# Performance work log

Hardware: AMD Instinct MI355X
Metric: run time of the kernel (lower is better)

## Reference

```python
import jax, jax.numpy as jnp
import numpy as np
from jax import lax

FEAT = 384        # features
FFN = 768         # ffn_features (chunk=True -> halves of 384)
ZDIM = FFN // 2   # 384
HID = 192         # AE hidden
B, N = 4, 128
LN_EPS = 1e-5


def gelu(x):
    return jax.nn.gelu(x, approximate=False)  # torch nn.GELU default = exact erf


def setup_inputs() -> dict:
    key = jax.random.key(0)
    ks = jax.random.split(key, 12)

    def lin(k, fan_in, shape):
        bound = 1.0 / np.sqrt(fan_in)
        return jax.random.uniform(k, shape, jnp.float32, -bound, bound)

    return {
        "x": jax.random.normal(ks[0], (B, N, FEAT), jnp.float32),
        "U_w": lin(ks[1], FEAT, (FEAT, FFN)),
        "U_b": lin(ks[2], FEAT, (FFN,)),
        "ln_w": jnp.ones((ZDIM,), jnp.float32),
        "ln_b": jnp.zeros((ZDIM,), jnp.float32),
        "enc_w": lin(ks[3], ZDIM, (ZDIM, HID)),
        "enc_b": lin(ks[4], ZDIM, (HID,)),
        "dec_w": lin(ks[5], HID, (HID, ZDIM)),
        "dec_b": lin(ks[6], HID, (ZDIM,)),
        "V_w": lin(ks[7], ZDIM, (ZDIM, FEAT)),
        "V_b": lin(ks[8], ZDIM, (FEAT,)),
    }


def _ae(z, enc_w, enc_b, dec_w, dec_b):
    h = gelu(z @ enc_w + enc_b)
    return h @ dec_w + dec_b


def reference(x, U_w, U_b, ln_w, ln_b, enc_w, enc_b, dec_w, dec_b, V_w, V_b):
    h = gelu(x @ U_w + U_b)                    # (B,N,FFN)
    xh, z = jnp.split(h, 2, axis=-1)           # chunk=True: (B,N,ZDIM) each
    z = lax.stop_gradient(z)                   # z.detach()
    mu = jnp.mean(z, axis=-1, keepdims=True)
    var = jnp.var(z, axis=-1, keepdims=True)
    z = (z - mu) / jnp.sqrt(var + LN_EPS) * ln_w + ln_b

    n = z.shape[1]
    eye = jnp.eye(n, dtype=z.dtype)
    # z_mask[b,i,j,:] = z[b,j,:] if i==j else 0   (mask_type='zeros')
    z_mask = eye[None, :, :, None] * z[:, None, :, :]   # (B,N,N,ZDIM)
    preds = _ae(z_mask, enc_w, enc_b, dec_w, dec_b)      # (B,N,N,ZDIM)
    dist = jnp.einsum('bijf,bjf->bij', preds, z)         # (B,N,N)
    attn = lax.stop_gradient(jax.nn.softmax(dist, axis=-1))
    out = jnp.einsum('bij,bjf->bif', attn, xh)           # (B,N,ZDIM)
    return out @ V_w + V_b                               # (B,N,FEAT)
```

## Files before the change

kernel.cpp:

```cpp
#include <hip/hip_runtime.h>
#include <hip/hip_bf16.h>
#include <math.h>

#define FEAT 384
#define FFN  768
#define ZDIM 384
#define HID  192
#define BB   4
#define NN   128
#define BN   (BB*NN)

__device__ __forceinline__ float gelu_exact(float x) {
    return 0.5f * x * (1.0f + erff(x * 0.70710678118654752440f));
}

__device__ __forceinline__ float bflo(unsigned u) { return __uint_as_float(u << 16); }
__device__ __forceinline__ float bfhi(unsigned u) { return __uint_as_float(u & 0xFFFF0000u); }

template<bool F32>
__device__ __forceinline__ float ldg(const void* p, int i) {
    if constexpr (F32) return ((const float*)p)[i];
    return __uint_as_float(((unsigned)((const unsigned short*)p)[i]) << 16);
}
template<bool F32>
__device__ __forceinline__ void stg(void* p, size_t i, float v) {
    if constexpr (F32) ((float*)p)[i] = v;
    else ((__hip_bfloat16*)p)[i] = __float2bfloat16(v);
}

template<bool F32> struct V4;
template<> struct V4<true> {
    float4 a;
    __device__ __forceinline__ void load(const void* p, size_t off) {
        a = *(const float4*)((const float*)p + off);
    }
    __device__ __forceinline__ float g(int i) const { return (&a.x)[i]; }
};
template<> struct V4<false> {
    uint2 u;
    __device__ __forceinline__ void load(const void* p, size_t off) {
        u = *(const uint2*)((const unsigned short*)p + off);
    }
    __device__ __forceinline__ float g(int i) const {
        const unsigned w = (&u.x)[i >> 1];
        return (i & 1) ? bfhi(w) : bflo(w);
    }
};

__device__ __forceinline__ bool is_f32(const void* ln_w) {
    return ((const unsigned short*)ln_w)[0] == 0;
}

__device__ __forceinline__ float block_sum(float v, float* sm) {
    for (int o = 32; o > 0; o >>= 1) v += __shfl_down(v, o, 64);
    const int lane = threadIdx.x & 63, w = threadIdx.x >> 6;
    __syncthreads();
    if (lane == 0) sm[w] = v;
    __syncthreads();
    return sm[0] + sm[1] + sm[2] + sm[3] + sm[4] + sm[5];
}
__device__ __forceinline__ float block_max(float v, float* sm) {
    for (int o = 32; o > 0; o >>= 1) v = fmaxf(v, __shfl_down(v, o, 64));
    const int lane = threadIdx.x & 63, w = threadIdx.x >> 6;
    __syncthreads();
    if (lane == 0) sm[w] = v;
    __syncthreads();
    return fmaxf(fmaxf(fmaxf(sm[0], sm[1]), fmaxf(sm[2], sm[3])), fmaxf(sm[4], sm[5]));
}
__device__ __forceinline__ void block_sum4(float v0, float v1, float v2, float v3,
                                           float* sm, float out[4]) {
    for (int o = 32; o > 0; o >>= 1) {
        v0 += __shfl_down(v0, o, 64);
        v1 += __shfl_down(v1, o, 64);
        v2 += __shfl_down(v2, o, 64);
        v3 += __shfl_down(v3, o, 64);
    }
    const int lane = threadIdx.x & 63, w = threadIdx.x >> 6;
    __syncthreads();
    if (lane == 0) { sm[w] = v0; sm[6 + w] = v1; sm[12 + w] = v2; sm[18 + w] = v3; }
    __syncthreads();
    #pragma unroll
    for (int q = 0; q < 4; q++)
        out[q] = sm[q*6] + sm[q*6+1] + sm[q*6+2] + sm[q*6+3] + sm[q*6+4] + sm[q*6+5];
}

#define SM_TOTAL 9816

template<bool F32, int KCH, int M>
__device__ __forceinline__ void gemmMx4(
    const void* __restrict__ W, int ldw, int c0, int kb,
    const float* __restrict__ in, int ldin, float acc[M][4])
{
    constexpr int NB = KCH / 8;
    V4<F32> buf[3][8];
    #pragma unroll
    for (int j = 0; j < 8; j++) buf[0][j].load(W, (size_t)(kb + j) * ldw + c0);
    if (NB > 1) {
        #pragma unroll
        for (int j = 0; j < 8; j++) buf[1][j].load(W, (size_t)(kb + 8 + j) * ldw + c0);
    }
    #pragma unroll
    for (int b = 0; b < NB; b++) {
        const int cur = b % 3;
        if (b + 2 < NB) {
            const int nxt = (b + 2) % 3;
            #pragma unroll
            for (int j = 0; j < 8; j++)
                buf[nxt][j].load(W, (size_t)(kb + (b + 2) * 8 + j) * ldw + c0);
        }
        #pragma unroll
        for (int m = 0; m < M; m++) {
            const float4 x0 = *(const float4*)(in + m * ldin + kb + b * 8);
            const float4 x1 = *(const float4*)(in + m * ldin + kb + b * 8 + 4);
            const float xv[8] = {x0.x, x0.y, x0.z, x0.w, x1.x, x1.y, x1.z, x1.w};
            #pragma unroll
            for (int j = 0; j < 8; j++) {
                #pragma unroll
                for (int i = 0; i < 4; i++)
                    acc[m][i] = fmaf(xv[j], buf[cur][j].g(i), acc[m][i]);
            }
        }
    }
}

template<bool F32>
__device__ void bodyA(float* S, int q,
    const void* __restrict__ x, const void* __restrict__ U_w,
    const void* __restrict__ U_b, const void* __restrict__ ln_w,
    const void* __restrict__ ln_b, const void* __restrict__ enc_w,
    const void* __restrict__ enc_b, const void* __restrict__ dec_w,
    const void* __restrict__ dec_b,
    float* __restrict__ d0, float* __restrict__ diag)
{
    const int rb = 4 * q;
    const int t = threadIdx.x;
    float* xs = S;
    float* zs = S + 1536;
    float* hid = S + 3072;
    float* gh = S + 3840;
    float* part = S + 4032;
    float* sm = S + 9792;

    #pragma unroll
    for (int m = 0; m < 4; m++) xs[m * 384 + t] = ldg<F32>(x, (rb + m) * FEAT + t);
    if (t < HID) gh[t] = gelu_exact(ldg<F32>(enc_b, t));
    __syncthreads();

    const int cg = t % 96, kh = t / 96;
    const int cL = 4 * cg, cG = ZDIM + cL, kb = 96 * kh;
    float acc[4][4] = {};
    gemmMx4<F32, 96, 4>(U_w, FFN, cG, kb, xs, 384, acc);
    if (kh > 0) {
        float* p = &part[(kh - 1) * 1536 + cg];
        #pragma unroll
        for (int m = 0; m < 4; m++)
            #pragma unroll
            for (int i = 0; i < 4; i++) p[(m * 4 + i) * 96] = acc[m][i];
    }
    __syncthreads();

    float hv[4][4];
    float s1[4] = {0,0,0,0}, s2[4] = {0,0,0,0};
    if (kh == 0) {
        #pragma unroll
        for (int i = 0; i < 4; i++) {
            const float ub = ldg<F32>(U_b, cG + i);
            #pragma unroll
            for (int m = 0; m < 4; m++) {
                float v = acc[m][i] + ub
                        + part[(m * 4 + i) * 96 + cg]
                        + part[1536 + (m * 4 + i) * 96 + cg]
                        + part[3072 + (m * 4 + i) * 96 + cg];
                v = gelu_exact(v);
                hv[m][i] = v;
                s1[m] += v; s2[m] += v * v;
            }
        }
    }
    float S1[4], S2[4];
    block_sum4(s1[0], s1[1], s1[2], s1[3], sm, S1);
    block_sum4(s2[0], s2[1], s2[2], s2[3], sm, S2);
    if (kh == 0) {
        #pragma unroll
        for (int m = 0; m < 4; m++) {
            const float mu = S1[m] * (1.0f / ZDIM);
            const float rs = rsqrtf(S2[m] * (1.0f / ZDIM) - mu * mu + 1e-5f);
            #pragma unroll
            for (int i = 0; i < 4; i++) {
                const int zc = cL + i;
                zs[m * 384 + zc] = (hv[m][i] - mu) * rs * ldg<F32>(ln_w, zc) + ldg<F32>(ln_b, zc);
            }
        }
    }
    __syncthreads();

    {
        const int cgE = t % 48, khE = t / 48;
        const int cE = 4 * cgE, kbE = 48 * khE;
        float ea[4][4] = {};
        gemmMx4<F32, 48, 4>(enc_w, HID, cE, kbE, zs, 384, ea);
        if (khE > 0) {
            float* p = &part[(khE - 1) * 768 + cgE];
            #pragma unroll
            for (int m = 0; m < 4; m++)
                #pragma unroll
                for (int i = 0; i < 4; i++) p[(m * 4 + i) * 48] = ea[m][i];
        }
        __syncthreads();
        if (khE == 0) {
            #pragma unroll
            for (int i = 0; i < 4; i++) {
                const float ebv = ldg<F32>(enc_b, cE + i);
                #pragma unroll
                for (int m = 0; m < 4; m++) {
                    float v = ea[m][i] + ebv;
                    #pragma unroll
                    for (int kk = 0; kk < 7; kk++)
                        v += part[kk * 768 + (m * 4 + i) * 48 + cgE];
                    hid[m * 192 + cE + i] = gelu_exact(v);
                }
            }
        }
        __syncthreads();
    }

    {
        const int cgD = t % 96, khD = t / 96;
        const int cD = 4 * cgD, kbD = 48 * khD;
        float da[5][4] = {};
        gemmMx4<F32, 48, 5>(dec_w, ZDIM, cD, kbD, hid, 192, da);
        if (khD > 0) {
            float* p = &part[(khD - 1) * 1920 + cgD];
            #pragma unroll
            for (int m = 0; m < 5; m++)
                #pragma unroll
                for (int i = 0; i < 4; i++) p[(m * 4 + i) * 96] = da[m][i];
        }
        __syncthreads();
        float pd[4] = {0,0,0,0}, pe[4] = {0,0,0,0};
        if (khD == 0) {
            #pragma unroll
            for (int i = 0; i < 4; i++) {
                const int c = cD + i;
                const float dbv = ldg<F32>(dec_b, c);
                float vc = da[4][i] + dbv;
                #pragma unroll
                for (int kk = 0; kk < 3; kk++)
                    vc += part[kk * 1920 + (16 + i) * 96 + cgD];
                #pragma unroll
                for (int m = 0; m < 4; m++) {
                    float v = da[m][i] + dbv;
                    #pragma unroll
                    for (int kk = 0; kk < 3; kk++)
                        v += part[kk * 1920 + (m * 4 + i) * 96 + cgD];
                    const float zv = zs[m * 384 + c];
                    pd[m] = fmaf(v, zv, pd[m]);
                    pe[m] = fmaf(vc, zv, pe[m]);
                }
            }
        }
        float DG[4], DD[4];
        block_sum4(pd[0], pd[1], pd[2], pd[3], sm, DG);
        block_sum4(pe[0], pe[1], pe[2], pe[3], sm, DD);
        if (t == 0) {
            #pragma unroll
            for (int m = 0; m < 4; m++) { diag[rb + m] = DG[m]; d0[rb + m] = DD[m]; }
        }
    }
}

template<bool F32>
__device__ void bodyB(float* S, int q,
    const void* __restrict__ x, const void* __restrict__ U_w,
    const void* __restrict__ U_b, const void* __restrict__ V_w,
    float* __restrict__ Y)
{
    const int rb = 4 * q;
    const int t = threadIdx.x;
    float* xs = S;
    float* zs = S + 1536;
    float* part = S + 4032;

    #pragma unroll
    for (int m = 0; m < 4; m++) xs[m * 384 + t] = ldg<F32>(x, (rb + m) * FEAT + t);
    __syncthreads();

    const int cg = t % 96, kh = t / 96;
    const int cL = 4 * cg, kb = 96 * kh;
    float acc[4][4] = {};
    gemmMx4<F32, 96, 4>(U_w, FFN, cL, kb, xs, 384, acc);
    if (kh > 0) {
        float* p = &part[(kh - 1) * 1536 + cg];
        #pragma unroll
        for (int m = 0; m < 4; m++)
            #pragma unroll
            for (int i = 0; i < 4; i++) p[(m * 4 + i) * 96] = acc[m][i];
    }
    __syncthreads();
    if (kh == 0) {
        #pragma unroll
        for (int i = 0; i < 4; i++) {
            const float ub = ldg<F32>(U_b, cL + i);
            #pragma unroll
            for (int m = 0; m < 4; m++) {
                float v = acc[m][i] + ub
                        + part[(m * 4 + i) * 96 + cg]
                        + part[1536 + (m * 4 + i) * 96 + cg]
                        + part[3072 + (m * 4 + i) * 96 + cg];
                zs[m * 384 + cL + i] = gelu_exact(v);
            }
        }
    }
    __syncthreads();

    float ya[4][4] = {};
    gemmMx4<F32, 96, 4>(V_w, FEAT, cL, kb, zs, 384, ya);
    if (kh > 0) {
        float* p = &part[(kh - 1) * 1536 + cg];
        #pragma unroll
        for (int m = 0; m < 4; m++)
            #pragma unroll
            for (int i = 0; i < 4; i++) p[(m * 4 + i) * 96] = ya[m][i];
    }
    __syncthreads();
    if (kh == 0) {
        #pragma unroll
        for (int m = 0; m < 4; m++) {
            float o[4];
            #pragma unroll
            for (int i = 0; i < 4; i++) {
                o[i] = ya[m][i]
                     + part[(m * 4 + i) * 96 + cg]
                     + part[1536 + (m * 4 + i) * 96 + cg]
                     + part[3072 + (m * 4 + i) * 96 + cg];
            }
            *(float4*)(Y + (size_t)(rb + m) * FEAT + cL) = make_float4(o[0], o[1], o[2], o[3]);
        }
    }
}

__global__ __launch_bounds__(384) void k_main(
    const void* x, const void* U_w, const void* U_b,
    const void* ln_w, const void* ln_b,
    const void* enc_w, const void* enc_b,
    const void* dec_w, const void* dec_b, const void* V_w,
    float* Y, float* d0, float* diag)
{
    __shared__ float S[SM_TOTAL];
    const int type = blockIdx.x & 1;
    const int q = blockIdx.x >> 1;
    if (is_f32(ln_w)) {
        if (type == 0) bodyA<true >(S, q, x, U_w, U_b, ln_w, ln_b, enc_w, enc_b, dec_w, dec_b, d0, diag);
        else           bodyB<true >(S, q, x, U_w, U_b, V_w, Y);
    } else {
        if (type == 0) bodyA<false>(S, q, x, U_w, U_b, ln_w, ln_b, enc_w, enc_b, dec_w, dec_b, d0, diag);
        else           bodyB<false>(S, q, x, U_w, U_b, V_w, Y);
    }
}

template<bool F32>
__device__ void combine_body(
    const float* __restrict__ d0, const float* __restrict__ diag,
    const float* __restrict__ Y,
    const void* __restrict__ V_b, void* __restrict__ out)
{
    const int b  = blockIdx.x >> 2;
    const int cc = (blockIdx.x & 3) * 96;
    const int t = threadIdx.x;
    const int c = t % 96, qq = t / 96;
    __shared__ float e0s[NN], eds[NN];
    __shared__ float bp[4 * 96];
    __shared__ float baseY[96];
    __shared__ float sm[12];

    float d0v = -INFINITY, dgv = -INFINITY;
    if (t < NN) { d0v = d0[b * NN + t]; dgv = diag[b * NN + t]; }
    const float m = block_max(fmaxf(d0v, dgv), sm);
    float e0v = 0.f;
    if (t < NN) {
        e0v = expf(d0v - m);
        e0s[t] = e0v;
        eds[t] = expf(dgv - m);
    }
    const float S = block_sum(e0v, sm);

    const float* Yb = Y + (size_t)b * NN * FEAT + cc + c;
    const int j0 = 32 * qq;
    float p = 0.f;
    for (int jj = 0; jj < 32; jj += 8) {
        float w[8];
        #pragma unroll
        for (int j = 0; j < 8; j++) w[j] = Yb[(size_t)(j0 + jj + j) * FEAT];
        #pragma unroll
        for (int j = 0; j < 8; j++) p = fmaf(e0s[j0 + jj + j], w[j], p);
    }
    bp[qq * 96 + c] = p;
    __syncthreads();
    if (qq == 0) baseY[c] = bp[c] + bp[96 + c] + bp[192 + c] + bp[288 + c];
    __syncthreads();

    const float bY = baseY[c];
    const float vb = ldg<F32>(V_b, cc + c);
    for (int rr = 0; rr < 32; rr += 8) {
        float w[8];
        #pragma unroll
        for (int j = 0; j < 8; j++) w[j] = Yb[(size_t)(j0 + rr + j) * FEAT];
        #pragma unroll
        for (int j = 0; j < 8; j++) {
            const int r = j0 + rr + j;
            const float inv = 1.0f / (S - e0s[r] + eds[r]);
            const float val = (bY + (eds[r] - e0s[r]) * w[j]) * inv + vb;
            stg<F32>(out, (size_t)(b * NN + r) * FEAT + cc + c, val);
        }
    }
}

__global__ __launch_bounds__(384) void k_combine(
    const void* ln_w,
    const float* d0, const float* diag, const float* Y,
    const void* V_b, void* out)
{
    if (is_f32(ln_w))
        combine_body<true >(d0, diag, Y, V_b, out);
    else
        combine_body<false>(d0, diag, Y, V_b, out);
}

extern "C" void kernel_launch(void* const* d_in, const int* in_sizes, int n_in,
                              void* d_out, int out_size, void* d_ws, size_t ws_size,
                              hipStream_t stream) {
    const void* x     = d_in[0];
    const void* U_w   = d_in[1];
    const void* U_b   = d_in[2];
    const void* ln_w  = d_in[3];
    const void* ln_b  = d_in[4];
    const void* enc_w = d_in[5];
    const void* enc_b = d_in[6];
    const void* dec_w = d_in[7];
    const void* dec_b = d_in[8];
    const void* V_w   = d_in[9];
    const void* V_b   = d_in[10];

    float* ws   = (float*)d_ws;
    float* Y    = ws;
    float* d0   = Y + (size_t)BN * FEAT;
    float* diag = d0 + BN;

    k_main<<<2 * (BN / 4), 384, 0, stream>>>(x, U_w, U_b, ln_w, ln_b, enc_w, enc_b,
                                             dec_w, dec_b, V_w, Y, d0, diag);
    k_combine<<<4 * BB, 384, 0, stream>>>(ln_w, d0, diag, Y, V_b, d_out);
}
```

Measured before the change: 105.0 us.

## Merge paired block reductions and spread combine kernel over more blocks

Replaces each pair of four-value block reductions with a single eight-value reduction, which halves the barrier round-trips during LayerNorm statistics and the diag/d0 dot products. The combine kernel goes from 16 to 64 blocks, each owning 24 output columns with 16 row groups of 8 rows. Each thread now loads its 8 Y values once and keeps them in registers, instead of reading Y a second time. The cost is narrower 24-float column accesses per row, which coalesce less well, and a 16-way partial sum in shared memory.

```diff
diff --git a/kernel.cpp b/kernel.cpp
--- a/kernel.cpp
+++ b/kernel.cpp
@@ -67,24 +67,27 @@
     __syncthreads();
     return fmaxf(fmaxf(fmaxf(sm[0], sm[1]), fmaxf(sm[2], sm[3])), fmaxf(sm[4], sm[5]));
 }
-__device__ __forceinline__ void block_sum4(float v0, float v1, float v2, float v3,
-                                           float* sm, float out[4]) {
+__device__ __forceinline__ void block_sum8(const float v[8], float* sm, float out[8]) {
+    float tv[8];
+    #pragma unroll
+    for (int n = 0; n < 8; n++) tv[n] = v[n];
     for (int o = 32; o > 0; o >>= 1) {
-        v0 += __shfl_down(v0, o, 64);
-        v1 += __shfl_down(v1, o, 64);
-        v2 += __shfl_down(v2, o, 64);
-        v3 += __shfl_down(v3, o, 64);
+        #pragma unroll
+        for (int n = 0; n < 8; n++) tv[n] += __shfl_down(tv[n], o, 64);
     }
     const int lane = threadIdx.x & 63, w = threadIdx.x >> 6;
     __syncthreads();
-    if (lane == 0) { sm[w] = v0; sm[6 + w] = v1; sm[12 + w] = v2; sm[18 + w] = v3; }
-    __syncthreads();
-    #pragma unroll
-    for (int q = 0; q < 4; q++)
-        out[q] = sm[q*6] + sm[q*6+1] + sm[q*6+2] + sm[q*6+3] + sm[q*6+4] + sm[q*6+5];
-}
-
-#define SM_TOTAL 9816
+    if (lane == 0) {
+        #pragma unroll
+        for (int n = 0; n < 8; n++) sm[n * 6 + w] = tv[n];
+    }
+    __syncthreads();
+    #pragma unroll
+    for (int n = 0; n < 8; n++)
+        out[n] = sm[n*6] + sm[n*6+1] + sm[n*6+2] + sm[n*6+3] + sm[n*6+4] + sm[n*6+5];
+}
+
+#define SM_TOTAL 9840
 
 template<bool F32, int KCH, int M>
 __device__ __forceinline__ void gemmMx4(
@@ -160,7 +163,7 @@
     __syncthreads();
 
     float hv[4][4];
-    float s1[4] = {0,0,0,0}, s2[4] = {0,0,0,0};
+    float sv[8] = {};
     if (kh == 0) {
         #pragma unroll
         for (int i = 0; i < 4; i++) {
@@ -173,18 +176,18 @@
                         + part[3072 + (m * 4 + i) * 96 + cg];
                 v = gelu_exact(v);
                 hv[m][i] = v;
-                s1[m] += v; s2[m] += v * v;
-            }
-        }
-    }
-    float S1[4], S2[4];
-    block_sum4(s1[0], s1[1], s1[2], s1[3], sm, S1);
-    block_sum4(s2[0], s2[1], s2[2], s2[3], sm, S2);
+                sv[m] += v;
+                sv[4 + m] += v * v;
+            }
+        }
+    }
+    float SS[8];
+    block_sum8(sv, sm, SS);
     if (kh == 0) {
         #pragma unroll
         for (int m = 0; m < 4; m++) {
-            const float mu = S1[m] * (1.0f / ZDIM);
-            const float rs = rsqrtf(S2[m] * (1.0f / ZDIM) - mu * mu + 1e-5f);
+            const float mu = SS[m] * (1.0f / ZDIM);
+            const float rs = rsqrtf(SS[4 + m] * (1.0f / ZDIM) - mu * mu + 1e-5f);
             #pragma unroll
             for (int i = 0; i < 4; i++) {
                 const int zc = cL + i;
@@ -237,7 +240,7 @@
                 for (int i = 0; i < 4; i++) p[(m * 4 + i) * 96] = da[m][i];
         }
         __syncthreads();
-        float pd[4] = {0,0,0,0}, pe[4] = {0,0,0,0};
+        float dv[8] = {};
         if (khD == 0) {
             #pragma unroll
             for (int i = 0; i < 4; i++) {
@@ -254,17 +257,16 @@
                     for (int kk = 0; kk < 3; kk++)
                         v += part[kk * 1920 + (m * 4 + i) * 96 + cgD];
                     const float zv = zs[m * 384 + c];
-                    pd[m] = fmaf(v, zv, pd[m]);
-                    pe[m] = fmaf(vc, zv, pe[m]);
+                    dv[m] = fmaf(v, zv, dv[m]);
+                    dv[4 + m] = fmaf(vc, zv, dv[4 + m]);
                 }
             }
         }
-        float DG[4], DD[4];
-        block_sum4(pd[0], pd[1], pd[2], pd[3], sm, DG);
-        block_sum4(pe[0], pe[1], pe[2], pe[3], sm, DD);
+        float DD8[8];
+        block_sum8(dv, sm, DD8);
         if (t == 0) {
             #pragma unroll
-            for (int m = 0; m < 4; m++) { diag[rb + m] = DG[m]; d0[rb + m] = DD[m]; }
+            for (int m = 0; m < 4; m++) { diag[rb + m] = DD8[m]; d0[rb + m] = DD8[4 + m]; }
         }
     }
 }
@@ -364,13 +366,13 @@
     const float* __restrict__ Y,
     const void* __restrict__ V_b, void* __restrict__ out)
 {
-    const int b  = blockIdx.x >> 2;
-    const int cc = (blockIdx.x & 3) * 96;
+    const int b  = blockIdx.x >> 4;
+    const int cc = (blockIdx.x & 15) * 24;
     const int t = threadIdx.x;
-    const int c = t % 96, qq = t / 96;
+    const int c = t % 24, qq = t / 24;
     __shared__ float e0s[NN], eds[NN];
-    __shared__ float bp[4 * 96];
-    __shared__ float baseY[96];
+    __shared__ float bp[16 * 24];
+    __shared__ float baseY[24];
     __shared__ float sm[12];
 
     float d0v = -INFINITY, dgv = -INFINITY;
@@ -385,33 +387,31 @@
     const float S = block_sum(e0v, sm);
 
     const float* Yb = Y + (size_t)b * NN * FEAT + cc + c;
-    const int j0 = 32 * qq;
+    const int j0 = 8 * qq;
+    float w[8];
+    #pragma unroll
+    for (int j = 0; j < 8; j++) w[j] = Yb[(size_t)(j0 + j) * FEAT];
     float p = 0.f;
-    for (int jj = 0; jj < 32; jj += 8) {
-        float w[8];
-        #pragma unroll
-        for (int j = 0; j < 8; j++) w[j] = Yb[(size_t)(j0 + jj + j) * FEAT];
-        #pragma unroll
-        for (int j = 0; j < 8; j++) p = fmaf(e0s[j0 + jj + j], w[j], p);
-    }
-    bp[qq * 96 + c] = p;
-    __syncthreads();
-    if (qq == 0) baseY[c] = bp[c] + bp[96 + c] + bp[192 + c] + bp[288 + c];
+    #pragma unroll
+    for (int j = 0; j < 8; j++) p = fmaf(e0s[j0 + j], w[j], p);
+    bp[qq * 24 + c] = p;
+    __syncthreads();
+    if (qq == 0) {
+        float s = 0.f;
+        #pragma unroll
+        for (int g = 0; g < 16; g++) s += bp[g * 24 + c];
+        baseY[c] = s;
+    }
     __syncthreads();
 
     const float bY = baseY[c];
     const float vb = ldg<F32>(V_b, cc + c);
-    for (int rr = 0; rr < 32; rr += 8) {
-        float w[8];
-        #pragma unroll
-        for (int j = 0; j < 8; j++) w[j] = Yb[(size_t)(j0 + rr + j) * FEAT];
-        #pragma unroll
-        for (int j = 0; j < 8; j++) {
-            const int r = j0 + rr + j;
-            const float inv = 1.0f / (S - e0s[r] + eds[r]);
-            const float val = (bY + (eds[r] - e0s[r]) * w[j]) * inv + vb;
-            stg<F32>(out, (size_t)(b * NN + r) * FEAT + cc + c, val);
-        }
+    #pragma unroll
+    for (int j = 0; j < 8; j++) {
+        const int r = j0 + j;
+        const float inv = 1.0f / (S - e0s[r] + eds[r]);
+        const float val = (bY + (eds[r] - e0s[r]) * w[j]) * inv + vb;
+        stg<F32>(out, (size_t)(b * NN + r) * FEAT + cc + c, val);
     }
 }
 
@@ -448,5 +448,5 @@
 
     k_main<<<2 * (BN / 4), 384, 0, stream>>>(x, U_w, U_b, ln_w, ln_b, enc_w, enc_b,
                                              dec_w, dec_b, V_w, Y, d0, diag);
-    k_combine<<<4 * BB, 384, 0, stream>>>(ln_w, d0, diag, Y, V_b, d_out);
-}
+    k_combine<<<16 * BB, 384, 0, stream>>>(ln_w, d0, diag, Y, V_b, d_out);
+}
```

New measurement: 102.0 us. -2.9%, faster.
